# Kernel optimization log

Measured on AMD Instinct MI355X. Metric: run time of the kernel, lower is better.

The kernel has to match this reference:

```python
import jax, jax.numpy as jnp
import numpy as np

# ---- static config (mirrors ConvCapsules init + assumed ConvCaps1 input) ----
KERNEL, STRIDE = 3, 2
CHILD_SPACE, CHILD_CAPS = 14, 32
PARENT_CAPS, ROUTINGS = 32, 3
BATCH = 8
FINAL_LAMBDA = 0.01
EPS = 1e-9
PARENT_SPACE = (CHILD_SPACE - KERNEL) // STRIDE + 1  # 6
P2 = PARENT_SPACE ** 2   # 36
KK = KERNEL ** 2         # 9
C2 = CHILD_SPACE ** 2    # 196


def _child_index_map():
    # For each parent spatial position p and kernel offset k (row-major, as
    # produced by kernel_tile's depthwise-conv trick), the flat child spatial
    # index. Also counts how many parents each child spatial position feeds.
    idx = np.zeros((P2, KK), dtype=np.int32)
    cnt = np.zeros((C2,), dtype=np.float32)
    for r in range(PARENT_SPACE):
        for c in range(PARENT_SPACE):
            p = r * PARENT_SPACE + c
            for i in range(KERNEL):
                for j in range(KERNEL):
                    s = (r * STRIDE + i) * CHILD_SPACE + (c * STRIDE + j)
                    idx[p, i * KERNEL + j] = s
                    cnt[s] += 1.0
    return idx, cnt

CHILD_IDX, PARENTS_PER_CHILD = _child_index_map()


def setup_inputs() -> dict:
    key = jax.random.key(0)
    k1, k2, k3, k4 = jax.random.split(key, 4)
    # last dim 17 = 16 pose + 1 activation; activation must be >= 0
    inputs = jax.random.uniform(k1, (BATCH, CHILD_SPACE, CHILD_SPACE, CHILD_CAPS, 17), dtype=jnp.float32)
    w = jax.random.normal(k2, (KK * CHILD_CAPS, PARENT_CAPS, 4, 4), dtype=jnp.float32)
    beta_v = jax.random.normal(k3, (1, 1, 1, PARENT_CAPS, 1), dtype=jnp.float32)
    beta_a = jax.random.normal(k4, (1, 1, 1, PARENT_CAPS, 1), dtype=jnp.float32)
    return {"inputs": inputs, "w": w, "beta_v": beta_v, "beta_a": beta_a}


def _kernel_tile(x):
    # x: [N,H,W,caps,A] -> [N, ps, ps, kk, caps, A]  (im2col gather)
    row = (np.arange(PARENT_SPACE) * STRIDE)[:, None] + np.arange(KERNEL)[None, :]  # (ps,k)
    x = x[:, row]             # [N, ps, k, W, caps, A]
    x = x[:, :, :, row]       # [N, ps, k, ps, k, caps, A]
    x = jnp.transpose(x, (0, 1, 3, 2, 4, 5, 6))  # [N, ps, ps, k, k, caps, A]
    return x.reshape(x.shape[0], PARENT_SPACE, PARENT_SPACE, KK, x.shape[-2], x.shape[-1])


def _em_routing(votes, act_i, beta_v, beta_a):
    # votes: [N, P2, KK*ci, o, 16]; act_i: [N, P2, KK*ci, 1, 1]
    N = votes.shape[0]
    ci, o = CHILD_CAPS, PARENT_CAPS
    flat_idx = CHILD_IDX.reshape(-1)  # (P2*KK,)

    # rr init: uniform over all parents (spatial x caps) each child routes to
    ppc = PARENTS_PER_CHILD[CHILD_IDX]  # (P2, KK)
    rr = jnp.asarray((1.0 / (ppc * o)).astype(np.float32))[None, :, :, None, None]
    rr = jnp.broadcast_to(rr, (1, P2, KK, ci, o)).reshape(1, P2, KK * ci, o, 1)

    for it in range(ROUTINGS):
        inv_temp = FINAL_LAMBDA * (1.0 - 0.95 ** (it + 1))
        # ---------------- M-step ----------------
        rr_prime = rr * act_i                                   # [N,P2,KK*ci,o,1]
        rr_sum = jnp.sum(rr_prime, axis=2, keepdims=True)       # [N,P2,1,o,1]
        mean = jnp.sum(rr_prime * votes, axis=2, keepdims=True) / (rr_sum + EPS)  # [N,P2,1,o,16]
        var = jnp.sum(rr_prime * (votes - mean) ** 2, axis=2, keepdims=True) / (rr_sum + EPS) + EPS
        cost_h = (beta_v + 0.5 * jnp.log(var)) * rr_sum          # [N,P2,1,o,16]
        cost = jnp.sum(cost_h, axis=-1, keepdims=True)           # [N,P2,1,o,1]
        cost_mean = jnp.mean(cost, axis=3, keepdims=True)
        cost_stdv = jnp.sqrt(jnp.sum((cost - cost_mean) ** 2, axis=3, keepdims=True) / o)
        act_j = jax.nn.sigmoid(inv_temp * (beta_a + (cost_mean - cost) / (cost_stdv + EPS)))
        if it < ROUTINGS - 1:
            # ---------------- E-step ----------------
            ln_p = (-0.5 * jnp.sum(jnp.log(2.0 * jnp.pi * var), axis=-1, keepdims=True)
                    - jnp.sum((votes - mean) ** 2 / (2.0 * var), axis=-1, keepdims=True))  # [N,P2,KK*ci,o,1]
            zz = jnp.log(act_j + EPS) + ln_p
            zz5 = zz.reshape(N, P2, KK, ci, o)
            # stable softmax over ALL parents (spatial positions x parent caps)
            # of each child, done sparsely via scatter-max / scatter-add keyed
            # on child spatial index
            zmax = jnp.max(zz5, axis=-1).reshape(N, P2 * KK, ci)
            cmax = jnp.full((N, C2, ci), -1e30, zz5.dtype).at[:, flat_idx, :].max(zmax)
            cmax = jax.lax.stop_gradient(cmax)
            e = jnp.exp(zz5 - cmax[:, CHILD_IDX][..., None])     # [N,P2,KK,ci,o]
            denom = jnp.zeros((N, C2, ci), zz5.dtype).at[:, flat_idx, :].add(
                jnp.sum(e, axis=-1).reshape(N, P2 * KK, ci))
            rr = (e / (denom[:, CHILD_IDX][..., None] + EPS)).reshape(N, P2, KK * ci, o, 1)

    pose_out = mean.reshape(N, PARENT_SPACE, PARENT_SPACE, o, 16)
    act_out = act_j.reshape(N, PARENT_SPACE, PARENT_SPACE, o, 1)
    return pose_out, act_out


def reference(inputs, w, beta_v, beta_a):
    N = inputs.shape[0]
    pose = inputs[..., :16]
    act = inputs[..., 16:]
    pose_t = _kernel_tile(pose)  # [N,ps,ps,KK,ci,16]
    act_t = _kernel_tile(act)    # [N,ps,ps,KK,ci,1]
    pose_u = pose_t.reshape(N * P2, KK * CHILD_CAPS, 4, 4)
    act_u = act_t.reshape(N, P2, KK * CHILD_CAPS, 1, 1)
    # votes: each child's 4x4 pose times learned 4x4 transform per parent cap
    votes = jnp.einsum('nkab,kobc->nkoac', pose_u, w)  # [N*P2, KK*ci, o, 4, 4]
    votes = votes.reshape(N, P2, KK * CHILD_CAPS, PARENT_CAPS, 16)
    pose_out, act_out = _em_routing(votes, act_u, beta_v, beta_a)
    return jnp.concatenate([act_out, pose_out], axis=-1)  # [N,ps,ps,o,17]
```

## Files before the change

kernel.cpp:

```cpp
#include <hip/hip_runtime.h>
#include <math.h>

#define PS 6
#define P2 36
#define CI 32
#define OO 32
#define KC 288
#define KCO 9216
#define EPSF 1e-9f
#define LOG2PI_F 1.8378770664093455f

#define ZZ_OFF   0u
#define WT_OFF   2654208u
#define PART_OFF 2801664u
#define MS_OFF   4018176u

__device__ __forceinline__ int covr(int x){
  int cnt = 0;
#pragma unroll
  for (int r = 0; r < 6; ++r) { int i = x - 2*r; cnt += (i >= 0 && i <= 2) ? 1 : 0; }
  return cnt;
}

__global__ __launch_bounds__(256) void wtrans_kernel(const float* __restrict__ w,
                                                     float* __restrict__ wT)
{
  int e = blockIdx.x * 256 + threadIdx.x;
  int b = e & 3, o = (e >> 2) & 31, c = (e >> 7) & 3, k = e >> 9;
  wT[e] = w[k*512 + o*16 + b*4 + c];
}

template<bool FIRST>
__global__ __launch_bounds__(256, 5) void moments_kernel(
    const float* __restrict__ inp, const float* __restrict__ wT,
    const float* __restrict__ zzg, const float2* __restrict__ msg,
    float* __restrict__ part)
{
  __shared__ float s_pose[72*16];
  __shared__ float s_m[72];
  __shared__ float s_s[72];
  __shared__ float s_red[4*1056];

  const int blk = blockIdx.x;
  const int np = blk >> 2, k4 = blk & 3;
  const int n = np / P2, p = np % P2;
  const int pr = p / PS, pc = p % PS;
  const int t = threadIdx.x;
  const int k0 = k4 * 72;

  const float* ibase = inp + (size_t)n * (196*32*17);
  for (int e = t; e < 72*16; e += 256) {
    int kl = e >> 4, h = e & 15;
    int k = k0 + kl;
    int kk = k >> 5, ci = k & 31;
    s_pose[e] = ibase[(((pr*2 + kk/3)*14 + (pc*2 + kk%3))*32 + ci)*17 + h];
  }
  if (t < 72) {
    int k = k0 + t; int kk = k >> 5, ci = k & 31;
    int x = pr*2 + kk/3, y = pc*2 + kk%3;
    if (FIRST) {
      float a = ibase[((x*14 + y)*32 + ci)*17 + 16];
      s_m[t] = a / (float)(covr(x) * covr(y) * OO);
    } else {
      float2 ms = msg[((size_t)(n*169 + x*13 + y))*32 + ci];
      s_m[t] = ms.x;
      s_s[t] = ms.y;
    }
  }
  __syncthreads();

  const int q = t >> 5, o = t & 31;
  float srr = 0.f;
  float m1[16], m2[16];
#pragma unroll
  for (int j = 0; j < 16; ++j) { m1[j] = 0.f; m2[j] = 0.f; }

  const float* zp = zzg + (size_t)np * KCO + ((size_t)k0 << 5) + o;

#pragma unroll 3
  for (int ks = 0; ks < 9; ++ks) {
    int kl = q*9 + ks;
    float rra;
    if (FIRST) rra = s_m[kl];
    else       rra = __expf(zp[(size_t)kl << 5] - s_m[kl]) * s_s[kl];
    const float4* pk  = (const float4*)s_pose + (kl << 2);
    const float4* wkb = (const float4*)wT + ((size_t)(k0 + kl) << 7) + o;
    float4 w0 = wkb[0], w1 = wkb[32], w2 = wkb[64], w3 = wkb[96];
    srr += rra;
#pragma unroll
    for (int a = 0; a < 4; ++a) {
      float4 A = pk[a];
      float v0 = A.x*w0.x + A.y*w0.y + A.z*w0.z + A.w*w0.w;
      float v1 = A.x*w1.x + A.y*w1.y + A.z*w1.z + A.w*w1.w;
      float v2 = A.x*w2.x + A.y*w2.y + A.z*w2.z + A.w*w2.w;
      float v3 = A.x*w3.x + A.y*w3.y + A.z*w3.z + A.w*w3.w;
      float r0 = rra*v0, r1 = rra*v1, r2 = rra*v2, r3 = rra*v3;
      m1[a*4+0] += r0;    m1[a*4+1] += r1;    m1[a*4+2] += r2;    m1[a*4+3] += r3;
      m2[a*4+0] += r0*v0; m2[a*4+1] += r1*v1; m2[a*4+2] += r2*v2; m2[a*4+3] += r3*v3;
    }
  }

  srr += __shfl_xor(srr, 32, 64);
#pragma unroll
  for (int j = 0; j < 16; ++j) {
    m1[j] += __shfl_xor(m1[j], 32, 64);
    m2[j] += __shfl_xor(m2[j], 32, 64);
  }
  {
    const int lane = t & 63, wv = t >> 6;
    if (lane < 32) {
      float* rb = s_red + wv*1056 + lane*33;
      rb[0] = srr;
#pragma unroll
      for (int j = 0; j < 16; ++j) { rb[1+j] = m1[j]; rb[17+j] = m2[j]; }
    }
  }
  __syncthreads();
  float* pb = part + (size_t)blk * 1056;
  for (int u = t; u < 1056; u += 256) {
    pb[u] = s_red[u] + s_red[1056+u] + s_red[2112+u] + s_red[3168+u];
  }
}

template<int IT>
__global__ __launch_bounds__(512, 4) void zzstats_kernel(
    const float* __restrict__ inp, const float* __restrict__ wT,
    const float* __restrict__ part,
    const float* __restrict__ beta_v, const float* __restrict__ beta_a,
    float* __restrict__ zzg)
{
  __shared__ float s_pose[72*16];
  __shared__ float s_mean[512];
  __shared__ float s_i2v[512];
  __shared__ float s_cost[OO];
  __shared__ float s_lvs[OO];
  __shared__ float s_lc[OO];

  const int blk = blockIdx.x;
  const int np = blk >> 2, k4 = blk & 3;
  const int n = np / P2, p = np % P2;
  const int pr = p / PS, pc = p % PS;
  const int t = threadIdx.x;
  const int k0 = k4 * 72;

  const float* ibase = inp + (size_t)n * (196*32*17);
  for (int e = t; e < 72*16; e += 512) {
    int kl = e >> 4, h = e & 15;
    int k = k0 + kl;
    int kk = k >> 5, ci = k & 31;
    s_pose[e] = ibase[(((pr*2 + kk/3)*14 + (pc*2 + kk%3))*32 + ci)*17 + h];
  }

  {
    const int so = t >> 4, h = t & 15;
    const float* pb = part + (size_t)np * 4224 + so*33;
    float rs = pb[0]    + pb[1056]      + pb[2112]      + pb[3168];
    float a1 = pb[1+h]  + pb[1056+1+h]  + pb[2112+1+h]  + pb[3168+1+h];
    float a2 = pb[17+h] + pb[1056+17+h] + pb[2112+17+h] + pb[3168+17+h];
    float S    = rs + EPSF;
    float mean = a1 / S;
    float var  = fmaxf(a2 / S - mean*mean, 0.f) + EPSF;
    float lvh  = __logf(var);
    float ch   = (beta_v[so] + 0.5f * lvh) * rs;
    float lv   = lvh;
#pragma unroll
    for (int d = 1; d < 16; d <<= 1) {
      ch += __shfl_xor(ch, d, 64);
      lv += __shfl_xor(lv, d, 64);
    }
    s_mean[t] = mean;
    s_i2v[t]  = 0.5f / var;
    if (h == 0) { s_cost[so] = ch; s_lvs[so] = lv; }
  }
  __syncthreads();

  if (t < OO) {
    float cm = 0.f;
#pragma unroll
    for (int oi = 0; oi < OO; ++oi) cm += s_cost[oi];
    cm *= (1.f / OO);
    float ssq = 0.f;
#pragma unroll
    for (int oi = 0; oi < OO; ++oi) { float d = s_cost[oi] - cm; ssq += d*d; }
    float sd = sqrtf(ssq * (1.f / OO));
    const float INVT = (IT==0) ? 5.0e-4f : 9.75e-4f;
    float arg = INVT * (beta_a[t] + (cm - s_cost[t]) / (sd + EPSF));
    float aj  = 1.f / (1.f + __expf(-arg));
    s_lc[t] = __logf(aj + EPSF) - 0.5f * (s_lvs[t] + 16.f * LOG2PI_F);
  }
  __syncthreads();

  {
    const int oz = t & 31;
    const int tq = t >> 5;
    const float lc = s_lc[oz];
    const float4* mo4 = (const float4*)(s_mean + (oz << 4));
    const float4* io4 = (const float4*)(s_i2v  + (oz << 4));
    float4 M0 = mo4[0], M1 = mo4[1], M2 = mo4[2], M3 = mo4[3];
    float4 I0 = io4[0], I1 = io4[1], I2 = io4[2], I3 = io4[3];
    float* zb = zzg + (size_t)np * KCO + ((size_t)k0 << 5);

    float4 w0n, w1n, w2n, w3n;
    {
      const float4* wkb = (const float4*)wT + ((size_t)(k0 + tq) << 7) + oz;
      w0n = wkb[0]; w1n = wkb[32]; w2n = wkb[64]; w3n = wkb[96];
    }
#pragma unroll
    for (int i = 0; i < 5; ++i) {
      if (i == 4 && tq >= 8) break;
      const int kl = (i < 4) ? (i*16 + tq) : (64 + tq);
      float4 w0 = w0n, w1 = w1n, w2 = w2n, w3 = w3n;
      if (i < 4) {
        int kln = (i < 3) ? (kl + 16) : (64 + (tq & 7));
        const float4* wkb = (const float4*)wT + ((size_t)(k0 + kln) << 7) + oz;
        w0n = wkb[0]; w1n = wkb[32]; w2n = wkb[64]; w3n = wkb[96];
      }
      const float4* pk = (const float4*)s_pose + (kl << 2);
      float ssum = 0.f;
      float4 A;
      A = pk[0];
      {
        float x0 = A.x*w0.x + A.y*w0.y + A.z*w0.z + A.w*w0.w;
        float x1 = A.x*w1.x + A.y*w1.y + A.z*w1.z + A.w*w1.w;
        float x2 = A.x*w2.x + A.y*w2.y + A.z*w2.z + A.w*w2.w;
        float x3 = A.x*w3.x + A.y*w3.y + A.z*w3.z + A.w*w3.w;
        float d0 = x0-M0.x, d1 = x1-M0.y, d2 = x2-M0.z, d3 = x3-M0.w;
        ssum += d0*d0*I0.x + d1*d1*I0.y + d2*d2*I0.z + d3*d3*I0.w;
      }
      A = pk[1];
      {
        float x0 = A.x*w0.x + A.y*w0.y + A.z*w0.z + A.w*w0.w;
        float x1 = A.x*w1.x + A.y*w1.y + A.z*w1.z + A.w*w1.w;
        float x2 = A.x*w2.x + A.y*w2.y + A.z*w2.z + A.w*w2.w;
        float x3 = A.x*w3.x + A.y*w3.y + A.z*w3.z + A.w*w3.w;
        float d0 = x0-M1.x, d1 = x1-M1.y, d2 = x2-M1.z, d3 = x3-M1.w;
        ssum += d0*d0*I1.x + d1*d1*I1.y + d2*d2*I1.z + d3*d3*I1.w;
      }
      A = pk[2];
      {
        float x0 = A.x*w0.x + A.y*w0.y + A.z*w0.z + A.w*w0.w;
        float x1 = A.x*w1.x + A.y*w1.y + A.z*w1.z + A.w*w1.w;
        float x2 = A.x*w2.x + A.y*w2.y + A.z*w2.z + A.w*w2.w;
        float x3 = A.x*w3.x + A.y*w3.y + A.z*w3.z + A.w*w3.w;
        float d0 = x0-M2.x, d1 = x1-M2.y, d2 = x2-M2.z, d3 = x3-M2.w;
        ssum += d0*d0*I2.x + d1*d1*I2.y + d2*d2*I2.z + d3*d3*I2.w;
      }
      A = pk[3];
      {
        float x0 = A.x*w0.x + A.y*w0.y + A.z*w0.z + A.w*w0.w;
        float x1 = A.x*w1.x + A.y*w1.y + A.z*w1.z + A.w*w1.w;
        float x2 = A.x*w2.x + A.y*w2.y + A.z*w2.z + A.w*w2.w;
        float x3 = A.x*w3.x + A.y*w3.y + A.z*w3.z + A.w*w3.w;
        float d0 = x0-M3.x, d1 = x1-M3.y, d2 = x2-M3.z, d3 = x3-M3.w;
        ssum += d0*d0*I3.x + d1*d1*I3.y + d2*d2*I3.z + d3*d3*I3.w;
      }
      zb[(kl << 5) + oz] = lc - ssum;
    }
  }
}

__global__ __launch_bounds__(512) void statsout_kernel(
    const float* __restrict__ part,
    const float* __restrict__ beta_v, const float* __restrict__ beta_a,
    float* __restrict__ out)
{
  __shared__ float s_cost[OO];
  const int np = blockIdx.x;
  const int t = threadIdx.x;
  const int o = t >> 4, h = t & 15;

  const float* pb = part + (size_t)np * 4224 + o*33;
  float rs = pb[0]    + pb[1056]      + pb[2112]      + pb[3168];
  float a1 = pb[1+h]  + pb[1056+1+h]  + pb[2112+1+h]  + pb[3168+1+h];
  float a2 = pb[17+h] + pb[1056+17+h] + pb[2112+17+h] + pb[3168+17+h];
  float S = rs + EPSF;
  float mean = a1 / S;
  float var  = fmaxf(a2 / S - mean*mean, 0.f) + EPSF;
  float ch   = (beta_v[o] + 0.5f * __logf(var)) * rs;
#pragma unroll
  for (int d = 1; d < 16; d <<= 1) ch += __shfl_xor(ch, d, 64);
  if (h == 0) s_cost[o] = ch;
  __syncthreads();

  float cm = 0.f;
#pragma unroll
  for (int oi = 0; oi < OO; ++oi) cm += s_cost[oi];
  cm *= (1.f / OO);
  float ssq = 0.f;
#pragma unroll
  for (int oi = 0; oi < OO; ++oi) { float d = s_cost[oi] - cm; ssq += d*d; }
  float sd = sqrtf(ssq * (1.f / OO));
  float arg = 1.42625e-3f * (beta_a[o] + (cm - s_cost[o]) / (sd + EPSF));
  float aj  = 1.f / (1.f + __expf(-arg));

  out[((size_t)np*OO + o)*17 + 1 + h] = mean;
  if (h == 0) out[((size_t)np*OO + o)*17] = aj;
}

__global__ __launch_bounds__(256) void childnorm_kernel(
    const float* __restrict__ inp, const float* __restrict__ zzg,
    float2* __restrict__ msg)
{
  const int tg = blockIdx.x * 256 + threadIdx.x;
  const int g = tg >> 2, slot = tg & 3;
  const int n   = g / (169*32);
  const int rem = g % (169*32);
  const int sc  = rem >> 5, ci = rem & 31;
  const int x = sc / 13, y = sc % 13;

  int base = -1; int cnt = 0;
#pragma unroll
  for (int r = 0; r < 6; ++r) {
    int i = x - 2*r;
    if (i < 0 || i > 2) continue;
#pragma unroll
    for (int c2 = 0; c2 < 6; ++c2) {
      int j = y - 2*c2;
      if (j < 0 || j > 2) continue;
      if (cnt == slot) base = (((n*P2 + r*6+c2)*9 + i*3+j)*CI + ci) << 5;
      ++cnt;
    }
  }

  const float4* z4 = (base >= 0) ? (const float4*)(zzg + base) : (const float4*)zzg;
  float4 zv[8];
#pragma unroll
  for (int q = 0; q < 8; ++q) zv[q] = z4[q];

  float m = -1e30f;
  if (base >= 0) {
#pragma unroll
    for (int q = 0; q < 8; ++q) {
      float4 v = zv[q];
      m = fmaxf(m, fmaxf(fmaxf(v.x, v.y), fmaxf(v.z, v.w)));
    }
  }
  m = fmaxf(m, __shfl_xor(m, 1, 64));
  m = fmaxf(m, __shfl_xor(m, 2, 64));

  float den = 0.f;
  if (base >= 0) {
#pragma unroll
    for (int q = 0; q < 8; ++q) {
      float4 v = zv[q];
      den += __expf(v.x-m) + __expf(v.y-m) + __expf(v.z-m) + __expf(v.w-m);
    }
  }
  den += __shfl_xor(den, 1, 64);
  den += __shfl_xor(den, 2, 64);

  if (slot == 0) {
    const float act = inp[(((size_t)n*196 + x*14 + y)*32 + ci)*17 + 16];
    float2 ms; ms.x = m; ms.y = act / (den + EPSF);
    msg[g] = ms;
  }
}

extern "C" void kernel_launch(void* const* d_in, const int* in_sizes, int n_in,
                              void* d_out, int out_size, void* d_ws, size_t ws_size,
                              hipStream_t stream)
{
  (void)in_sizes; (void)n_in; (void)out_size; (void)ws_size;
  const float* inp = (const float*)d_in[0];
  const float* w   = (const float*)d_in[1];
  const float* bv  = (const float*)d_in[2];
  const float* ba  = (const float*)d_in[3];
  float* out = (float*)d_out;
  float* ws  = (float*)d_ws;
  float* zz   = ws + ZZ_OFF;
  float* wT   = ws + WT_OFF;
  float* part = ws + PART_OFF;
  float2* msg = (float2*)(ws + MS_OFF);

  wtrans_kernel<<<576, 256, 0, stream>>>(w, wT);

  moments_kernel<true ><<<1152, 256, 0, stream>>>(inp, wT, zz, msg, part);
  zzstats_kernel<0><<<1152, 512, 0, stream>>>(inp, wT, part, bv, ba, zz);
  childnorm_kernel<<<676, 256, 0, stream>>>(inp, zz, msg);

  moments_kernel<false><<<1152, 256, 0, stream>>>(inp, wT, zz, msg, part);
  zzstats_kernel<1><<<1152, 512, 0, stream>>>(inp, wT, part, bv, ba, zz);
  childnorm_kernel<<<676, 256, 0, stream>>>(inp, zz, msg);

  moments_kernel<false><<<1152, 256, 0, stream>>>(inp, wT, zz, msg, part);
  statsout_kernel<<<288, 512, 0, stream>>>(part, bv, ba, out);
}
```

Before: 114.6 us.

## Split stats from zz computation and use finer 8-way k-split blocks

The moments and zz kernels now split each parent position's 288 child votes into eight 36-vote blocks of 128 threads instead of four 72-vote blocks. The per-parent statistics (mean, inverse variance, log coefficient) are computed once per parent in a new 288-block stats kernel and written to workspace, instead of being recomputed redundantly in every zz block. This is meant to remove duplicated stats work and improve load balance and occupancy. In exchange it adds two extra kernel launches and global round trips for the stats, drops the weight register prefetching in the zz loop, and makes the partial-sum reduction read 8 slices.

```diff
diff --git a/kernel.cpp b/kernel.cpp
--- a/kernel.cpp
+++ b/kernel.cpp
@@ -13,7 +13,10 @@
 #define ZZ_OFF   0u
 #define WT_OFF   2654208u
 #define PART_OFF 2801664u
-#define MS_OFF   4018176u
+#define MEAN_OFF 5234688u
+#define I2V_OFF  5382144u
+#define LC_OFF   5529600u
+#define MS_OFF   5538816u
 
 __device__ __forceinline__ int covr(int x){
   int cnt = 0;
@@ -31,31 +34,31 @@
 }
 
 template<bool FIRST>
-__global__ __launch_bounds__(256, 5) void moments_kernel(
+__global__ __launch_bounds__(128) void moments_kernel(
     const float* __restrict__ inp, const float* __restrict__ wT,
     const float* __restrict__ zzg, const float2* __restrict__ msg,
     float* __restrict__ part)
 {
-  __shared__ float s_pose[72*16];
-  __shared__ float s_m[72];
-  __shared__ float s_s[72];
-  __shared__ float s_red[4*1056];
+  __shared__ float s_pose[36*16];
+  __shared__ float s_m[36];
+  __shared__ float s_s[36];
+  __shared__ float s_red[2*1056];
 
   const int blk = blockIdx.x;
-  const int np = blk >> 2, k4 = blk & 3;
+  const int np = blk >> 3, k8 = blk & 7;
   const int n = np / P2, p = np % P2;
   const int pr = p / PS, pc = p % PS;
   const int t = threadIdx.x;
-  const int k0 = k4 * 72;
+  const int k0 = k8 * 36;
 
   const float* ibase = inp + (size_t)n * (196*32*17);
-  for (int e = t; e < 72*16; e += 256) {
+  for (int e = t; e < 36*16; e += 128) {
     int kl = e >> 4, h = e & 15;
     int k = k0 + kl;
     int kk = k >> 5, ci = k & 31;
     s_pose[e] = ibase[(((pr*2 + kk/3)*14 + (pc*2 + kk%3))*32 + ci)*17 + h];
   }
-  if (t < 72) {
+  if (t < 36) {
     int k = k0 + t; int kk = k >> 5, ci = k & 31;
     int x = pr*2 + kk/3, y = pc*2 + kk%3;
     if (FIRST) {
@@ -117,184 +120,145 @@
   }
   __syncthreads();
   float* pb = part + (size_t)blk * 1056;
-  for (int u = t; u < 1056; u += 256) {
-    pb[u] = s_red[u] + s_red[1056+u] + s_red[2112+u] + s_red[3168+u];
+  for (int u = t; u < 1056; u += 128) {
+    pb[u] = s_red[u] + s_red[1056+u];
   }
 }
 
 template<int IT>
-__global__ __launch_bounds__(512, 4) void zzstats_kernel(
-    const float* __restrict__ inp, const float* __restrict__ wT,
+__global__ __launch_bounds__(512) void statsmid_kernel(
     const float* __restrict__ part,
     const float* __restrict__ beta_v, const float* __restrict__ beta_a,
-    float* __restrict__ zzg)
-{
-  __shared__ float s_pose[72*16];
-  __shared__ float s_mean[512];
-  __shared__ float s_i2v[512];
+    float* __restrict__ meang, float* __restrict__ i2vg, float* __restrict__ lcg,
+    float* __restrict__ out)
+{
   __shared__ float s_cost[OO];
   __shared__ float s_lvs[OO];
-  __shared__ float s_lc[OO];
-
+  const int np = blockIdx.x;
+  const int t = threadIdx.x;
+  const int so = t >> 4, h = t & 15;
+
+  const float* pb = part + (size_t)np * 8448 + so*33;
+  float rs = 0.f, a1 = 0.f, a2 = 0.f;
+#pragma unroll
+  for (int g = 0; g < 8; ++g) {
+    const float* qb = pb + g*1056;
+    rs += qb[0]; a1 += qb[1+h]; a2 += qb[17+h];
+  }
+  float S    = rs + EPSF;
+  float mean = a1 / S;
+  float var  = fmaxf(a2 / S - mean*mean, 0.f) + EPSF;
+  float lvh  = __logf(var);
+  float ch   = (beta_v[so] + 0.5f * lvh) * rs;
+  float lv   = lvh;
+#pragma unroll
+  for (int d = 1; d < 16; d <<= 1) {
+    ch += __shfl_xor(ch, d, 64);
+    lv += __shfl_xor(lv, d, 64);
+  }
+  if (IT == 2) {
+    out[((size_t)np*OO + so)*17 + 1 + h] = mean;
+  } else {
+    meang[(size_t)np*512 + t] = mean;
+    i2vg[(size_t)np*512 + t] = 0.5f / var;
+  }
+  if (h == 0) { s_cost[so] = ch; s_lvs[so] = lv; }
+  __syncthreads();
+
+  if (t < OO) {
+    float cm = 0.f;
+#pragma unroll
+    for (int oi = 0; oi < OO; ++oi) cm += s_cost[oi];
+    cm *= (1.f / OO);
+    float ssq = 0.f;
+#pragma unroll
+    for (int oi = 0; oi < OO; ++oi) { float d = s_cost[oi] - cm; ssq += d*d; }
+    float sd = sqrtf(ssq * (1.f / OO));
+    const float INVT = (IT==0) ? 5.0e-4f : ((IT==1) ? 9.75e-4f : 1.42625e-3f);
+    float arg = INVT * (beta_a[t] + (cm - s_cost[t]) / (sd + EPSF));
+    float aj  = 1.f / (1.f + __expf(-arg));
+    if (IT == 2) out[((size_t)np*OO + t)*17] = aj;
+    else lcg[(size_t)np*OO + t] = __logf(aj + EPSF) - 0.5f * (s_lvs[t] + 16.f * LOG2PI_F);
+  }
+}
+
+__global__ __launch_bounds__(128) void zz_kernel(
+    const float* __restrict__ inp, const float* __restrict__ wT,
+    const float* __restrict__ meang, const float* __restrict__ i2vg,
+    const float* __restrict__ lcg, float* __restrict__ zzg)
+{
+  __shared__ float s_pose[36*16];
   const int blk = blockIdx.x;
-  const int np = blk >> 2, k4 = blk & 3;
+  const int np = blk >> 3, k8 = blk & 7;
   const int n = np / P2, p = np % P2;
   const int pr = p / PS, pc = p % PS;
   const int t = threadIdx.x;
-  const int k0 = k4 * 72;
+  const int k0 = k8 * 36;
 
   const float* ibase = inp + (size_t)n * (196*32*17);
-  for (int e = t; e < 72*16; e += 512) {
+  for (int e = t; e < 36*16; e += 128) {
     int kl = e >> 4, h = e & 15;
     int k = k0 + kl;
     int kk = k >> 5, ci = k & 31;
     s_pose[e] = ibase[(((pr*2 + kk/3)*14 + (pc*2 + kk%3))*32 + ci)*17 + h];
   }
-
-  {
-    const int so = t >> 4, h = t & 15;
-    const float* pb = part + (size_t)np * 4224 + so*33;
-    float rs = pb[0]    + pb[1056]      + pb[2112]      + pb[3168];
-    float a1 = pb[1+h]  + pb[1056+1+h]  + pb[2112+1+h]  + pb[3168+1+h];
-    float a2 = pb[17+h] + pb[1056+17+h] + pb[2112+17+h] + pb[3168+17+h];
-    float S    = rs + EPSF;
-    float mean = a1 / S;
-    float var  = fmaxf(a2 / S - mean*mean, 0.f) + EPSF;
-    float lvh  = __logf(var);
-    float ch   = (beta_v[so] + 0.5f * lvh) * rs;
-    float lv   = lvh;
-#pragma unroll
-    for (int d = 1; d < 16; d <<= 1) {
-      ch += __shfl_xor(ch, d, 64);
-      lv += __shfl_xor(lv, d, 64);
-    }
-    s_mean[t] = mean;
-    s_i2v[t]  = 0.5f / var;
-    if (h == 0) { s_cost[so] = ch; s_lvs[so] = lv; }
-  }
   __syncthreads();
 
-  if (t < OO) {
-    float cm = 0.f;
-#pragma unroll
-    for (int oi = 0; oi < OO; ++oi) cm += s_cost[oi];
-    cm *= (1.f / OO);
-    float ssq = 0.f;
-#pragma unroll
-    for (int oi = 0; oi < OO; ++oi) { float d = s_cost[oi] - cm; ssq += d*d; }
-    float sd = sqrtf(ssq * (1.f / OO));
-    const float INVT = (IT==0) ? 5.0e-4f : 9.75e-4f;
-    float arg = INVT * (beta_a[t] + (cm - s_cost[t]) / (sd + EPSF));
-    float aj  = 1.f / (1.f + __expf(-arg));
-    s_lc[t] = __logf(aj + EPSF) - 0.5f * (s_lvs[t] + 16.f * LOG2PI_F);
-  }
-  __syncthreads();
-
-  {
-    const int oz = t & 31;
-    const int tq = t >> 5;
-    const float lc = s_lc[oz];
-    const float4* mo4 = (const float4*)(s_mean + (oz << 4));
-    const float4* io4 = (const float4*)(s_i2v  + (oz << 4));
-    float4 M0 = mo4[0], M1 = mo4[1], M2 = mo4[2], M3 = mo4[3];
-    float4 I0 = io4[0], I1 = io4[1], I2 = io4[2], I3 = io4[3];
-    float* zb = zzg + (size_t)np * KCO + ((size_t)k0 << 5);
-
-    float4 w0n, w1n, w2n, w3n;
+  const int oz = t & 31;
+  const int tq = t >> 5;
+  const float lc = lcg[(size_t)np*OO + oz];
+  const float4* mo4 = (const float4*)(meang + (size_t)np*512 + (oz << 4));
+  const float4* io4 = (const float4*)(i2vg  + (size_t)np*512 + (oz << 4));
+  float4 M0 = mo4[0], M1 = mo4[1], M2 = mo4[2], M3 = mo4[3];
+  float4 I0 = io4[0], I1 = io4[1], I2 = io4[2], I3 = io4[3];
+  float* zb = zzg + (size_t)np * KCO + ((size_t)k0 << 5);
+
+#pragma unroll 3
+  for (int i = 0; i < 9; ++i) {
+    const int kl = i*4 + tq;
+    const float4* wkb = (const float4*)wT + ((size_t)(k0 + kl) << 7) + oz;
+    float4 w0 = wkb[0], w1 = wkb[32], w2 = wkb[64], w3 = wkb[96];
+    const float4* pk = (const float4*)s_pose + (kl << 2);
+    float ssum = 0.f;
+    float4 A;
+    A = pk[0];
     {
-      const float4* wkb = (const float4*)wT + ((size_t)(k0 + tq) << 7) + oz;
-      w0n = wkb[0]; w1n = wkb[32]; w2n = wkb[64]; w3n = wkb[96];
-    }
-#pragma unroll
-    for (int i = 0; i < 5; ++i) {
-      if (i == 4 && tq >= 8) break;
-      const int kl = (i < 4) ? (i*16 + tq) : (64 + tq);
-      float4 w0 = w0n, w1 = w1n, w2 = w2n, w3 = w3n;
-      if (i < 4) {
-        int kln = (i < 3) ? (kl + 16) : (64 + (tq & 7));
-        const float4* wkb = (const float4*)wT + ((size_t)(k0 + kln) << 7) + oz;
-        w0n = wkb[0]; w1n = wkb[32]; w2n = wkb[64]; w3n = wkb[96];
-      }
-      const float4* pk = (const float4*)s_pose + (kl << 2);
-      float ssum = 0.f;
-      float4 A;
-      A = pk[0];
-      {
-        float x0 = A.x*w0.x + A.y*w0.y + A.z*w0.z + A.w*w0.w;
-        float x1 = A.x*w1.x + A.y*w1.y + A.z*w1.z + A.w*w1.w;
-        float x2 = A.x*w2.x + A.y*w2.y + A.z*w2.z + A.w*w2.w;
-        float x3 = A.x*w3.x + A.y*w3.y + A.z*w3.z + A.w*w3.w;
-        float d0 = x0-M0.x, d1 = x1-M0.y, d2 = x2-M0.z, d3 = x3-M0.w;
-        ssum += d0*d0*I0.x + d1*d1*I0.y + d2*d2*I0.z + d3*d3*I0.w;
-      }
-      A = pk[1];
-      {
-        float x0 = A.x*w0.x + A.y*w0.y + A.z*w0.z + A.w*w0.w;
-        float x1 = A.x*w1.x + A.y*w1.y + A.z*w1.z + A.w*w1.w;
-        float x2 = A.x*w2.x + A.y*w2.y + A.z*w2.z + A.w*w2.w;
-        float x3 = A.x*w3.x + A.y*w3.y + A.z*w3.z + A.w*w3.w;
-        float d0 = x0-M1.x, d1 = x1-M1.y, d2 = x2-M1.z, d3 = x3-M1.w;
-        ssum += d0*d0*I1.x + d1*d1*I1.y + d2*d2*I1.z + d3*d3*I1.w;
-      }
-      A = pk[2];
-      {
-        float x0 = A.x*w0.x + A.y*w0.y + A.z*w0.z + A.w*w0.w;
-        float x1 = A.x*w1.x + A.y*w1.y + A.z*w1.z + A.w*w1.w;
-        float x2 = A.x*w2.x + A.y*w2.y + A.z*w2.z + A.w*w2.w;
-        float x3 = A.x*w3.x + A.y*w3.y + A.z*w3.z + A.w*w3.w;
-        float d0 = x0-M2.x, d1 = x1-M2.y, d2 = x2-M2.z, d3 = x3-M2.w;
-        ssum += d0*d0*I2.x + d1*d1*I2.y + d2*d2*I2.z + d3*d3*I2.w;
-      }
-      A = pk[3];
-      {
-        float x0 = A.x*w0.x + A.y*w0.y + A.z*w0.z + A.w*w0.w;
-        float x1 = A.x*w1.x + A.y*w1.y + A.z*w1.z + A.w*w1.w;
-        float x2 = A.x*w2.x + A.y*w2.y + A.z*w2.z + A.w*w2.w;
-        float x3 = A.x*w3.x + A.y*w3.y + A.z*w3.z + A.w*w3.w;
-        float d0 = x0-M3.x, d1 = x1-M3.y, d2 = x2-M3.z, d3 = x3-M3.w;
-        ssum += d0*d0*I3.x + d1*d1*I3.y + d2*d2*I3.z + d3*d3*I3.w;
-      }
-      zb[(kl << 5) + oz] = lc - ssum;
-    }
-  }
-}
-
-__global__ __launch_bounds__(512) void statsout_kernel(
-    const float* __restrict__ part,
-    const float* __restrict__ beta_v, const float* __restrict__ beta_a,
-    float* __restrict__ out)
-{
-  __shared__ float s_cost[OO];
-  const int np = blockIdx.x;
-  const int t = threadIdx.x;
-  const int o = t >> 4, h = t & 15;
-
-  const float* pb = part + (size_t)np * 4224 + o*33;
-  float rs = pb[0]    + pb[1056]      + pb[2112]      + pb[3168];
-  float a1 = pb[1+h]  + pb[1056+1+h]  + pb[2112+1+h]  + pb[3168+1+h];
-  float a2 = pb[17+h] + pb[1056+17+h] + pb[2112+17+h] + pb[3168+17+h];
-  float S = rs + EPSF;
-  float mean = a1 / S;
-  float var  = fmaxf(a2 / S - mean*mean, 0.f) + EPSF;
-  float ch   = (beta_v[o] + 0.5f * __logf(var)) * rs;
-#pragma unroll
-  for (int d = 1; d < 16; d <<= 1) ch += __shfl_xor(ch, d, 64);
-  if (h == 0) s_cost[o] = ch;
-  __syncthreads();
-
-  float cm = 0.f;
-#pragma unroll
-  for (int oi = 0; oi < OO; ++oi) cm += s_cost[oi];
-  cm *= (1.f / OO);
-  float ssq = 0.f;
-#pragma unroll
-  for (int oi = 0; oi < OO; ++oi) { float d = s_cost[oi] - cm; ssq += d*d; }
-  float sd = sqrtf(ssq * (1.f / OO));
-  float arg = 1.42625e-3f * (beta_a[o] + (cm - s_cost[o]) / (sd + EPSF));
-  float aj  = 1.f / (1.f + __expf(-arg));
-
-  out[((size_t)np*OO + o)*17 + 1 + h] = mean;
-  if (h == 0) out[((size_t)np*OO + o)*17] = aj;
+      float x0 = A.x*w0.x + A.y*w0.y + A.z*w0.z + A.w*w0.w;
+      float x1 = A.x*w1.x + A.y*w1.y + A.z*w1.z + A.w*w1.w;
+      float x2 = A.x*w2.x + A.y*w2.y + A.z*w2.z + A.w*w2.w;
+      float x3 = A.x*w3.x + A.y*w3.y + A.z*w3.z + A.w*w3.w;
+      float d0 = x0-M0.x, d1 = x1-M0.y, d2 = x2-M0.z, d3 = x3-M0.w;
+      ssum += d0*d0*I0.x + d1*d1*I0.y + d2*d2*I0.z + d3*d3*I0.w;
+    }
+    A = pk[1];
+    {
+      float x0 = A.x*w0.x + A.y*w0.y + A.z*w0.z + A.w*w0.w;
+      float x1 = A.x*w1.x + A.y*w1.y + A.z*w1.z + A.w*w1.w;
+      float x2 = A.x*w2.x + A.y*w2.y + A.z*w2.z + A.w*w2.w;
+      float x3 = A.x*w3.x + A.y*w3.y + A.z*w3.z + A.w*w3.w;
+      float d0 = x0-M1.x, d1 = x1-M1.y, d2 = x2-M1.z, d3 = x3-M1.w;
+      ssum += d0*d0*I1.x + d1*d1*I1.y + d2*d2*I1.z + d3*d3*I1.w;
+    }
+    A = pk[2];
+    {
+      float x0 = A.x*w0.x + A.y*w0.y + A.z*w0.z + A.w*w0.w;
+      float x1 = A.x*w1.x + A.y*w1.y + A.z*w1.z + A.w*w1.w;
+      float x2 = A.x*w2.x + A.y*w2.y + A.z*w2.z + A.w*w2.w;
+      float x3 = A.x*w3.x + A.y*w3.y + A.z*w3.z + A.w*w3.w;
+      float d0 = x0-M2.x, d1 = x1-M2.y, d2 = x2-M2.z, d3 = x3-M2.w;
+      ssum += d0*d0*I2.x + d1*d1*I2.y + d2*d2*I2.z + d3*d3*I2.w;
+    }
+    A = pk[3];
+    {
+      float x0 = A.x*w0.x + A.y*w0.y + A.z*w0.z + A.w*w0.w;
+      float x1 = A.x*w1.x + A.y*w1.y + A.z*w1.z + A.w*w1.w;
+      float x2 = A.x*w2.x + A.y*w2.y + A.z*w2.z + A.w*w2.w;
+      float x3 = A.x*w3.x + A.y*w3.y + A.z*w3.z + A.w*w3.w;
+      float d0 = x0-M3.x, d1 = x1-M3.y, d2 = x2-M3.z, d3 = x3-M3.w;
+      ssum += d0*d0*I3.x + d1*d1*I3.y + d2*d2*I3.z + d3*d3*I3.w;
+    }
+    zb[(kl << 5) + oz] = lc - ssum;
+  }
 }
 
 __global__ __launch_bounds__(256) void childnorm_kernel(
@@ -367,21 +331,26 @@
   const float* ba  = (const float*)d_in[3];
   float* out = (float*)d_out;
   float* ws  = (float*)d_ws;
-  float* zz   = ws + ZZ_OFF;
-  float* wT   = ws + WT_OFF;
-  float* part = ws + PART_OFF;
-  float2* msg = (float2*)(ws + MS_OFF);
+  float* zz    = ws + ZZ_OFF;
+  float* wT    = ws + WT_OFF;
+  float* part  = ws + PART_OFF;
+  float* meang = ws + MEAN_OFF;
+  float* i2vg  = ws + I2V_OFF;
+  float* lcg   = ws + LC_OFF;
+  float2* msg  = (float2*)(ws + MS_OFF);
 
   wtrans_kernel<<<576, 256, 0, stream>>>(w, wT);
 
-  moments_kernel<true ><<<1152, 256, 0, stream>>>(inp, wT, zz, msg, part);
-  zzstats_kernel<0><<<1152, 512, 0, stream>>>(inp, wT, part, bv, ba, zz);
+  moments_kernel<true ><<<2304, 128, 0, stream>>>(inp, wT, zz, msg, part);
+  statsmid_kernel<0><<<288, 512, 0, stream>>>(part, bv, ba, meang, i2vg, lcg, out);
+  zz_kernel<<<2304, 128, 0, stream>>>(inp, wT, meang, i2vg, lcg, zz);
   childnorm_kernel<<<676, 256, 0, stream>>>(inp, zz, msg);
 
-  moments_kernel<false><<<1152, 256, 0, stream>>>(inp, wT, zz, msg, part);
-  zzstats_kernel<1><<<1152, 512, 0, stream>>>(inp, wT, part, bv, ba, zz);
+  moments_kernel<false><<<2304, 128, 0, stream>>>(inp, wT, zz, msg, part);
+  statsmid_kernel<1><<<288, 512, 0, stream>>>(part, bv, ba, meang, i2vg, lcg, out);
+  zz_kernel<<<2304, 128, 0, stream>>>(inp, wT, meang, i2vg, lcg, zz);
   childnorm_kernel<<<676, 256, 0, stream>>>(inp, zz, msg);
 
-  moments_kernel<false><<<1152, 256, 0, stream>>>(inp, wT, zz, msg, part);
-  statsout_kernel<<<288, 512, 0, stream>>>(part, bv, ba, out);
-}
+  moments_kernel<false><<<2304, 128, 0, stream>>>(inp, wT, zz, msg, part);
+  statsmid_kernel<2><<<288, 512, 0, stream>>>(part, bv, ba, meang, i2vg, lcg, out);
+}
```

New measurement: 125.6 us. 1.1x slower.
